# Performance work log

Hardware: AMD Instinct MI355X
Metric: run time of the kernel (lower is better)

Reference implementation:

```python
import jax, jax.numpy as jnp
import numpy as np

NUM_NODES = 40000
NUM_REL = 474
ENT_DIM = 100
REL_DIM = 100
NHID = 100
NHEADS = 2
OUT_DIM = NHID * NHEADS  # 200
ALPHA = 0.2
NUM_ORTHO_HEADS = 2
ORTHO_LAMBDA = 0.01
EPS = 1e-12


def _l2norm(x):
    n = jnp.sqrt(jnp.sum(x * x, axis=1, keepdims=True))
    return x / jnp.maximum(n, EPS)


def _leaky_relu(x):
    return jnp.where(x >= 0, x, ALPHA * x)


def _ortho_loss(a):
    # orthogonality penalty between the NUM_ORTHO_HEADS row-blocks of `a`
    Af = a.reshape(NUM_ORTHO_HEADS, -1)
    Afn = Af / jnp.maximum(jnp.linalg.norm(Af, axis=1, keepdims=True), EPS)
    G = Afn @ Afn.T
    return ORTHO_LAMBDA * jnp.sum((G - jnp.eye(NUM_ORTHO_HEADS, dtype=a.dtype)) ** 2)


def _gat_layer(x, tgt, src, rel, a, a2, concat):
    # x: [N, f]; tgt/src: [E]; rel: [E, r]; a: [out, 2f+r]; a2: [out]
    f = x.shape[1]
    a_t, a_s, a_r = a[:, :f], a[:, f:2 * f], a[:, 2 * f:]
    # edge_m = a @ concat(x[tgt], x[src], rel)^T, computed without materializing the concat
    edge_m = x[tgt] @ a_t.T + x[src] @ a_s.T + rel @ a_r.T  # [E, out]
    powers = -_leaky_relu(edge_m @ a2)  # [E]
    edge_e = jnp.exp(powers)
    rowsum = jax.ops.segment_sum(edge_e, tgt, num_segments=NUM_NODES)  # [N]
    rowsum = jnp.where(rowsum == 0.0, EPS, rowsum)
    h = jax.ops.segment_sum(edge_e[:, None] * edge_m, tgt, num_segments=NUM_NODES)  # [N, out]
    h = h / rowsum[:, None]
    if concat:
        h = jax.nn.elu(h)
    return h, _ortho_loss(a)


def setup_inputs() -> dict:
    key = jax.random.key(0)
    ks = jax.random.split(key, 12)
    E, EN, B = 100000, 30000, 8192
    edge_list = jax.random.randint(ks[0], (2, E), 0, NUM_NODES)
    edge_type = jax.random.randint(ks[1], (E,), 0, NUM_REL)
    batch_inputs = jax.random.randint(ks[2], (B, 3), 0, NUM_REL)  # col 2 < 474 < NUM_NODES, valid node ids
    train_indices_nhop = jax.random.randint(ks[3], (EN, 4), 0, NUM_REL)
    s = 0.1
    entity_embeddings = jax.random.normal(ks[4], (NUM_NODES, ENT_DIM), jnp.float32)
    relation_embeddings = jax.random.normal(ks[5], (NUM_REL, REL_DIM), jnp.float32)
    W_entities = jax.random.normal(ks[6], (ENT_DIM, OUT_DIM), jnp.float32) * s
    W_rel = jax.random.normal(ks[7], (REL_DIM, OUT_DIM), jnp.float32) * s
    att_a = jax.random.normal(ks[8], (NHEADS, NHID, 2 * ENT_DIM + REL_DIM), jnp.float32) * s
    att_a2 = jax.random.normal(ks[9], (NHEADS, NHID), jnp.float32) * s
    out_a = jax.random.normal(ks[10], (OUT_DIM, 3 * OUT_DIM), jnp.float32) * s
    out_a2 = jax.random.normal(ks[11], (OUT_DIM,), jnp.float32) * s
    return {
        'edge_list': edge_list, 'edge_type': edge_type,
        'batch_inputs': batch_inputs, 'train_indices_nhop': train_indices_nhop,
        'entity_embeddings': entity_embeddings, 'relation_embeddings': relation_embeddings,
        'W_entities': W_entities, 'W_rel': W_rel,
        'att_a': att_a, 'att_a2': att_a2, 'out_a': out_a, 'out_a2': out_a2,
    }


def reference(edge_list, edge_type, batch_inputs, train_indices_nhop,
              entity_embeddings, relation_embeddings, W_entities, W_rel,
              att_a, att_a2, out_a, out_a2):
    ent = _l2norm(entity_embeddings)
    # edge lists: aggregation index is edge[0] (target); nhop edges = (col3, col0)
    tgt = jnp.concatenate([edge_list[0], train_indices_nhop[:, 3]])
    src = jnp.concatenate([edge_list[1], train_indices_nhop[:, 0]])
    # layer-1 relation features (1-hop gather + 2-hop sum fusion)
    rel1 = jnp.concatenate([
        relation_embeddings[edge_type],
        relation_embeddings[train_indices_nhop[:, 1]] + relation_embeddings[train_indices_nhop[:, 2]],
    ], axis=0)
    outs = []
    total_ortho = jnp.zeros((), dtype=ent.dtype)
    for i in range(NHEADS):
        h, ol = _gat_layer(ent, tgt, src, rel1, att_a[i], att_a2[i], True)
        outs.append(h)
        total_ortho = total_ortho + ol
    x = jnp.concatenate(outs, axis=1)  # [N, OUT_DIM]  (dropout skipped: eval mode)
    out_relation_1 = relation_embeddings @ W_rel  # [R, OUT_DIM]
    rel2 = jnp.concatenate([
        out_relation_1[edge_type],
        out_relation_1[train_indices_nhop[:, 1]] + out_relation_1[train_indices_nhop[:, 2]],
    ], axis=0)
    x, ol = _gat_layer(x, tgt, src, rel2, out_a, out_a2, False)
    total_ortho = total_ortho + ol
    mask = jnp.zeros((NUM_NODES,), dtype=x.dtype).at[batch_inputs[:, 2]].set(1.0)
    out_entity = ent @ W_entities + mask[:, None] * x
    out_entity = _l2norm(out_entity)
    return out_entity, out_relation_1, total_ortho
```

## Files before the change

### kernel.cpp

```cpp
#include <hip/hip_runtime.h>
#include <cstdint>
#include <cstddef>
#include <math.h>

#define N_NODES 40000
#define N_RELS  474
#define E0      100000
#define NE      130000
#define NB      8192
#define LRALPHA 0.2f

#define KP1 128
#define KP2 256
#define LD1 608
#define LD2 416
#define NPAD1 640
#define NPAD2 448
#define DTH 16

#define M1_L2N   2500
#define M1_HIST  (M1_L2N + 508)
#define M1_UVEC  (M1_HIST + 200)
#define M1_MASK  (M1_UVEC + 32)
#define M1_TOT   (M1_MASK + 128)
#define M2_PACK1 1
#define M2_PACK2 (M2_PACK1 + 320)
#define M2_TOT   (M2_PACK2 + 448)
#define M3_GEMM  508
#define M3_MM    (M3_GEMM + 1250)
#define M3_RELP  (M3_MM + 32)
#define M3_CMP   (M3_RELP + 119)
#define M3_TOT   (M3_CMP + 157)
#define M4_MM    119
#define M4_OFIN  (M4_MM + 32)
#define M4_TOT   (M4_OFIN + 1)
#define N1_MAIN  2500
#define N1_HUB   (N1_MAIN + 512)
#define N1_TOT   (N1_HUB + 119)
#define HUBW     2048
#define N2_MAIN  1250
#define N2_TOT   (N2_MAIN + 512)

typedef __attribute__((ext_vector_type(8))) short short8;
typedef __attribute__((ext_vector_type(4))) float floatx4;

static __device__ __forceinline__ unsigned short f2bf(float f) {
    union { float f; uint32_t u; } v; v.f = f;
    uint32_t r = v.u + 0x7fff + ((v.u >> 16) & 1);
    return (unsigned short)(r >> 16);
}
static __device__ __forceinline__ float bf2f(unsigned short h) {
    union { uint32_t u; float f; } v; v.u = ((uint32_t)h) << 16;
    return v.f;
}
static __device__ __forceinline__ float bflo(uint32_t u) { return bf2f((unsigned short)(u & 0xffff)); }
static __device__ __forceinline__ float bfhi(uint32_t u) { return bf2f((unsigned short)(u >> 16)); }

static __device__ __forceinline__ int rdl(int v, int l) {
    return __builtin_amdgcn_readlane(v, l);
}
static __device__ __forceinline__ float rdlf(float v, int l) {
    return __int_as_float(__builtin_amdgcn_readlane(__float_as_int(v), l));
}
static __device__ __forceinline__ float frcp(float x) { return __builtin_amdgcn_rcpf(x); }


static __device__ void d_l2norm(int bid, int tid, const float* __restrict__ in,
                                unsigned short* __restrict__ out) {
    int wid = (bid * 256 + tid) >> 6;
    int lane = tid & 63;
    int w0 = wid * 4;
    if (w0 >= N_NODES) return;
    int j1 = lane + 64;
    bool v1ok = (j1 < 100);
    float a[4], b[4];
#pragma unroll
    for (int i = 0; i < 4; i++) {
        const float* r = in + (size_t)(w0 + i) * 100;
        a[i] = r[lane];
        b[i] = v1ok ? r[j1] : 0.f;
    }
    float ss[4];
#pragma unroll
    for (int i = 0; i < 4; i++) ss[i] = a[i] * a[i] + b[i] * b[i];
#pragma unroll
    for (int o = 32; o > 0; o >>= 1) {
#pragma unroll
        for (int i = 0; i < 4; i++) ss[i] += __shfl_down(ss[i], o);
    }
#pragma unroll
    for (int i = 0; i < 4; i++) {
        float s = __shfl(ss[i], 0);
        float inv = 1.f / fmaxf(sqrtf(s), 1e-12f);
        unsigned short* dst = out + (size_t)(w0 + i) * KP1;
        dst[lane] = f2bf(a[i] * inv);
        dst[j1] = v1ok ? f2bf(b[i] * inv) : (unsigned short)0;
    }
}

static __device__ void d_hist(int bid, int tid, const int* __restrict__ tgt_el,
                              const int* __restrict__ nhop, int* __restrict__ deg) {
    int e = bid * 256 + tid;
    if (e >= NE) return;
    int t = (e < E0) ? tgt_el[e] : nhop[(size_t)(e - E0) * 4 + 3];
    atomicAdd(&deg[t], 1);
}

static __device__ void d_uvec(int bid, int tid, const float* __restrict__ att_a,
                              const float* __restrict__ att_a2, const float* __restrict__ out_a,
                              const float* __restrict__ out_a2, float* __restrict__ uvecs) {
    int g = (bid * 256 + tid) >> 6;
    int lane = tid & 63;
    if (g >= 800) return;
    float s = 0.f;
    if (g < 400) {
        int v = g / 100, k = g % 100;
        int head = v >> 1, part = v & 1;
        const float* base = att_a + head * 30000 + part * 100 + k;
        const float* a2 = att_a2 + head * 100;
        for (int n = lane; n < 100; n += 64) s += a2[n] * base[n * 300];
    } else {
        int v = (g - 400) / 200, k = (g - 400) % 200;
        const float* base = out_a + v * 200 + k;
        for (int n = lane; n < 200; n += 64) s += out_a2[n] * base[n * 600];
    }
#pragma unroll
    for (int o = 32; o > 0; o >>= 1) s += __shfl_down(s, o);
    if (lane == 0) uvecs[g] = s;
}

static __device__ void d_mask(int bid, int tid, const int* __restrict__ batch,
                              float* __restrict__ mask) {
    int i = bid * 256 + tid;
    if (i < NB) mask[batch[(size_t)i * 3 + 2]] = 1.0f;
}

static __device__ void d_ortho_part(int bid, int tid, const float* __restrict__ att_a,
                                    const float* __restrict__ out_a, float* __restrict__ accum) {
    float loc[9] = {0,0,0,0,0,0,0,0,0};
    for (int i = bid * 256 + tid; i < 90000; i += 128 * 256) {
        int seg, li;
        const float* base;
        int L;
        if (i < 15000)      { seg = 0; li = i;          base = att_a;         L = 15000; }
        else if (i < 30000) { seg = 1; li = i - 15000;  base = att_a + 30000; L = 15000; }
        else                { seg = 2; li = i - 30000;  base = out_a;         L = 60000; }
        float a = base[li], b = base[L + li];
        loc[seg * 3 + 0] += a * a;
        loc[seg * 3 + 1] += b * b;
        loc[seg * 3 + 2] += a * b;
    }
    int lane = tid & 63;
#pragma unroll
    for (int q = 0; q < 9; q++) {
        float s = loc[q];
#pragma unroll
        for (int o = 32; o > 0; o >>= 1) s += __shfl_down(s, o);
        if (lane == 0 && s != 0.f) atomicAdd(&accum[q], s);
    }
}

static __device__ void d_scan2(int tid, int* wtot, int* __restrict__ bsums, int nb) {
    int v = (tid < nb) ? bsums[tid] : 0;
    int lane = tid & 63, wv = tid >> 6;
    int x = v;
#pragma unroll
    for (int o = 1; o < 64; o <<= 1) {
        int t = __shfl_up(x, o);
        if (lane >= o) x += t;
    }
    if (lane == 63) wtot[wv] = x;
    __syncthreads();
    int add = 0;
    for (int k = 0; k < wv; k++) add += wtot[k];
    __syncthreads();
    if (tid < nb) bsums[tid] = add + x - v;
    if (tid == 255) bsums[nb] = add + x;
}

static __device__ void d_pack1(int bid, int tid, const float* __restrict__ att_a,
                               const float* __restrict__ W_ent, const float* __restrict__ uvecs,
                               unsigned short* __restrict__ W) {
    int idx = bid * 256 + tid;
    if (idx >= NPAD1 * KP1) return;
    int j = idx & 7;
    int lane = (idx >> 3) & 63;
    int u = idx >> 9;
    int ks = u & 3;
    int t = u >> 2;
    int r = t * 16 + (lane & 15);
    int k = ks * 32 + (lane >> 4) * 8 + j;
    float val = 0.f;
    if (k < 100) {
        if (r < 200) {
            int i = r >> 1, h = r & 1;
            val = att_a[h * 30000 + i * 300 + k];
        } else if (r < 400) {
            int rr = r - 200, i = rr >> 1, h = rr & 1;
            val = att_a[h * 30000 + i * 300 + 100 + k];
        } else if (r < 600) {
            val = W_ent[k * 200 + (r - 400)];
        } else if (r < 604) {
            val = uvecs[(r - 600) * 100 + k];
        }
    }
    W[idx] = f2bf(val);
}

static __device__ void d_pack2(int bid, int tid, const float* __restrict__ out_a,
                               const float* __restrict__ uvecs, unsigned short* __restrict__ W) {
    int idx = bid * 256 + tid;
    if (idx >= NPAD2 * KP2) return;
    int j = idx & 7;
    int lane = (idx >> 3) & 63;
    int u = idx >> 9;
    int ks = u & 7;
    int t = u >> 3;
    int r = t * 16 + (lane & 15);
    int k = ks * 32 + (lane >> 4) * 8 + j;
    float val = 0.f;
    if (k < 200) {
        int klog = (k & 1) * 100 + (k >> 1);
        if (r < 200)       val = out_a[r * 600 + klog];
        else if (r < 400)  val = out_a[(r - 200) * 600 + 200 + klog];
        else if (r == 400) val = uvecs[400 + klog];
        else if (r == 401) val = uvecs[600 + klog];
    }
    W[idx] = f2bf(val);
}

static __device__ void d_scatter(int bid, int tid, const int* __restrict__ tgt_el,
                                 const int* __restrict__ src_el, const int* __restrict__ etype,
                                 const int* __restrict__ nhop, int* __restrict__ cursor,
                                 int* __restrict__ srcs, int2* __restrict__ relpk) {
    int e = bid * 256 + tid;
    if (e >= NE) return;
    int t, s, r1, r2;
    if (e < E0) {
        t = tgt_el[e]; s = src_el[e]; r1 = etype[e]; r2 = -1;
    } else {
        const int* nh = nhop + (size_t)(e - E0) * 4;
        t = nh[3]; s = nh[0]; r1 = nh[1]; r2 = nh[2];
    }
    int p = atomicAdd(&cursor[t], 1);
    srcs[p] = s;
    relpk[p] = make_int2(r1, r2);
}

static __device__ void d_compact(int bid, int tid, const int* __restrict__ rowptr,
                                 const float* __restrict__ mask,
                                 int* __restrict__ Hlist, int* __restrict__ Mlist,
                                 int* __restrict__ cnts) {
    int i = bid * 256 + tid;
    if (i >= N_NODES) return;
    int deg = rowptr[i + 1] - rowptr[i];
    if (deg > DTH) { int p = atomicAdd(&cnts[0], 1); Hlist[p] = i; }
    if (mask[i] != 0.f) { int p = atomicAdd(&cnts[1], 1); Mlist[p] = i; }
}

template <int KP>
static __device__ void d_gemm(int bx, int by, char* smem_raw, int tid,
                              const unsigned short* __restrict__ A,
                              const unsigned short* __restrict__ B,
                              unsigned short* __restrict__ C,
                              int ldc, int N, int gPerSplit) {
    constexpr int KSTEPS = KP / 32;
    constexpr int KCH = KSTEPS / 4;
    unsigned short (*cbuf)[16][64] = (unsigned short (*)[16][64])smem_raw;
    int wave = tid >> 6;
    int lane = tid & 63;
    int quad = lane >> 4;
    int l16 = lane & 15;
    int m0 = bx * 64 + wave * 16;
    short8 afrag[KSTEPS];
    const unsigned short* arow = A + (size_t)(m0 + l16) * KP + quad * 8;
#pragma unroll
    for (int ks = 0; ks < KSTEPS; ks++)
        afrag[ks] = *(const short8*)(arow + ks * 32);

    int Gtot = (N + 63) >> 6;
    int g0 = by * gPerSplit;
    int g1 = g0 + gPerSplit;
    if (g1 > Gtot) g1 = Gtot;
    for (int g = g0; g < g1; g++) {
        int nb = g << 6;
        const unsigned short* bgrp = B + (((size_t)(g << 2) * KSTEPS) << 9) + (lane << 3);
        floatx4 acc[4];
#pragma unroll
        for (int t = 0; t < 4; t++) acc[t] = (floatx4){0.f, 0.f, 0.f, 0.f};
#pragma unroll
        for (int ch = 0; ch < KCH; ch++) {
            short8 bf[4][4];
#pragma unroll
            for (int t = 0; t < 4; t++)
#pragma unroll
                for (int k = 0; k < 4; k++)
                    bf[t][k] = *(const short8*)(bgrp + ((size_t)(t * KSTEPS + ch * 4 + k) << 9));
#pragma unroll
            for (int k = 0; k < 4; k++)
#pragma unroll
                for (int t = 0; t < 4; t++)
                    acc[t] = __builtin_amdgcn_mfma_f32_16x16x32_bf16(afrag[ch * 4 + k], bf[t][k], acc[t], 0, 0, 0);
        }
        int r0 = quad * 4;
#pragma unroll
        for (int t = 0; t < 4; t++)
#pragma unroll
            for (int i = 0; i < 4; i++)
                cbuf[wave][r0 + i][t * 16 + l16] = f2bf(acc[t][i]);
        int colsA = N - nb; if (colsA > 64) colsA = 64;
        int cols8 = colsA >> 3;
        int sh = (colsA >= 64) ? 3 : 2;
        int nchunks = cols8 << 4;
        for (int c = lane; c < nchunks; c += 64) {
            int row = c >> sh;
            int col8 = (c & (cols8 - 1)) << 3;
            *(uint4*)(C + (size_t)(m0 + row) * ldc + nb + col8) =
                *(const uint4*)&cbuf[wave][row][col8];
        }
    }
}

template <bool BT>
static __device__ void d_mm(int bx, int by, char* smem_raw, int tid,
                            const float* __restrict__ A, int lda,
                            const float* __restrict__ B, int ldb,
                            float* __restrict__ C, int ldc,
                            int M, int N, int K) {
    float (*As)[65] = (float (*)[65])smem_raw;
    float (*Bs)[65] = (float (*)[65])(smem_raw + 16 * 65 * 4);
    int tx = tid & 15, ty = tid >> 4;
    int m0 = by * 64, n0 = bx * 64;
    float acc[4][4] = {};
    for (int k0 = 0; k0 < K; k0 += 16) {
        {
            int r = tid >> 2;
            int c4 = (tid & 3) * 4;
            int m = m0 + r;
#pragma unroll
            for (int u = 0; u < 4; u++) {
                int k = k0 + c4 + u;
                As[c4 + u][r] = (m < M && k < K) ? A[(size_t)m * lda + k] : 0.f;
            }
        }
        if (BT) {
            int r = tid >> 2;
            int c4 = (tid & 3) * 4;
            int n = n0 + r;
#pragma unroll
            for (int u = 0; u < 4; u++) {
                int k = k0 + c4 + u;
                Bs[c4 + u][r] = (n < N && k < K) ? B[(size_t)n * ldb + k] : 0.f;
            }
        } else {
            int kk = tid >> 4;
            int nn4 = (tid & 15) * 4;
            int k = k0 + kk;
#pragma unroll
            for (int u = 0; u < 4; u++) {
                int n = n0 + nn4 + u;
                Bs[kk][nn4 + u] = (k < K && n < N) ? B[(size_t)k * ldb + n] : 0.f;
            }
        }
        __syncthreads();
#pragma unroll
        for (int k = 0; k < 16; k++) {
            float a[4], b[4];
#pragma unroll
            for (int i = 0; i < 4; i++) a[i] = As[k][ty + 16 * i];
#pragma unroll
            for (int j = 0; j < 4; j++) b[j] = Bs[k][tx + 16 * j];
#pragma unroll
            for (int i = 0; i < 4; i++)
#pragma unroll
                for (int j = 0; j < 4; j++) acc[i][j] += a[i] * b[j];
        }
        __syncthreads();
    }
#pragma unroll
    for (int i = 0; i < 4; i++) {
        int m = m0 + ty + 16 * i;
        if (m >= M) continue;
#pragma unroll
        for (int j = 0; j < 4; j++) {
            int n = n0 + tx + 16 * j;
            if (n < N) C[(size_t)m * ldc + n] = acc[i][j];
        }
    }
}

static __device__ void d_relproj1(int bid, int tid, const float* __restrict__ rel_emb,
                                  const float* __restrict__ att_a, float* __restrict__ R1i) {
    int w = (bid * 256 + tid) >> 6;
    int lane = tid & 63;
    if (w >= N_RELS) return;
    const float* re = rel_emb + (size_t)w * 100;
    float2* dst = (float2*)(R1i + (size_t)w * 200);
    for (int f = lane; f < 100; f += 64) {
        const float* a0 = att_a + f * 300 + 200;
        const float* a1 = att_a + 30000 + f * 300 + 200;
// ... 288 lines not shown
        uint32_t sq = *(const uint32_t*)(Qcat + (size_t)sL * LD2 + 400);
        float pp = tdot + bfhi(sq) + dr;
        pp = (pp >= 0.f) ? pp : LRALPHA * pp;
        WL = __expf(-pp);
    }
    float c0 = 0.f, c1 = 0.f, c2 = 0.f, c3 = 0.f;
    float rs = 0.f;
    for (int j = 0; j < fast; j += 4) {
#pragma unroll
        for (int u = 0; u < 4; u++) {
            int jj = j + u;
            bool act = (jj < fast);
            int ls = act ? jj : 0;
            int sE = rdl(sL, ls);
            int rxE = rdl(rxL, ls);
            int ryE = act ? rdl(ryL, ls) : -1;
            float WE = act ? rdlf(WL, ls) : 0.f;
            uint2 qv = make_uint2(0u, 0u);
            float4 rv = make_float4(0.f, 0.f, 0.f, 0.f);
            if (fv) {
                qv = *(const uint2*)(Qcat + (size_t)sE * LD2 + 200 + c4);
                rv = *(const float4*)(R2 + (size_t)rxE * 200 + c4);
                if (ryE >= 0) {
                    float4 rb = *(const float4*)(R2 + (size_t)ryE * 200 + c4);
                    rv.x += rb.x; rv.y += rb.y; rv.z += rb.z; rv.w += rb.w;
                }
            }
            rs += WE;
            c0 += WE * (bflo(qv.x) + rv.x);
            c1 += WE * (bfhi(qv.x) + rv.y);
            c2 += WE * (bflo(qv.y) + rv.z);
            c3 += WE * (bfhi(qv.y) + rv.w);
        }
    }
    for (int p = beg + 64; p < end; p++) {
        int sE = srcs[p];
        int2 rp = relpk[p];
        float dr = dR2[rp.x];
        if (rp.y >= 0) dr += dR2[rp.y];
        uint32_t sq = *(const uint32_t*)(Qcat + (size_t)sE * LD2 + 400);
        float pp = tdot + bfhi(sq) + dr;
        pp = (pp >= 0.f) ? pp : LRALPHA * pp;
        float W = __expf(-pp);
        uint2 qv = make_uint2(0u, 0u);
        float4 rv = make_float4(0.f, 0.f, 0.f, 0.f);
        if (fv) {
            qv = *(const uint2*)(Qcat + (size_t)sE * LD2 + 200 + c4);
            rv = *(const float4*)(R2 + (size_t)rp.x * 200 + c4);
            if (rp.y >= 0) {
                float4 rb = *(const float4*)(R2 + (size_t)rp.y * 200 + c4);
                rv.x += rb.x; rv.y += rb.y; rv.z += rb.z; rv.w += rb.w;
            }
        }
        rs += W;
        c0 += W * (bflo(qv.x) + rv.x);
        c1 += W * (bfhi(qv.x) + rv.y);
        c2 += W * (bflo(qv.y) + rv.z);
        c3 += W * (bfhi(qv.y) + rv.w);
    }
    float d = (rs == 0.f) ? 1e-12f : rs;
    float idn = frcp(d);
    float mk = mask[node];
    float val0 = 0.f, val1 = 0.f, val2 = 0.f, val3 = 0.f;
    if (fv) {
        uint2 t = *(const uint2*)(Qcat + (size_t)node * LD2 + c4);
        uint2 e = *(const uint2*)(Pcat + (size_t)node * LD1 + 400 + c4);
        val0 = bflo(e.x) + mk * ((c0 + rs * bflo(t.x)) * idn);
        val1 = bfhi(e.x) + mk * ((c1 + rs * bfhi(t.x)) * idn);
        val2 = bflo(e.y) + mk * ((c2 + rs * bflo(t.y)) * idn);
        val3 = bfhi(e.y) + mk * ((c3 + rs * bfhi(t.y)) * idn);
    }
    float ss = val0 * val0 + val1 * val1 + val2 * val2 + val3 * val3;
#pragma unroll
    for (int o = 32; o > 0; o >>= 1) ss += __shfl_down(ss, o);
    ss = __shfl(ss, 0);
    float inv = frcp(fmaxf(sqrtf(ss), 1e-12f));
    if (fv) {
        *(float4*)(out + (size_t)node * 200 + c4) =
            make_float4(val0 * inv, val1 * inv, val2 * inv, val3 * inv);
    }
}


__global__ __launch_bounds__(256) void k_mega1(
        const float* __restrict__ ent_emb, unsigned short* __restrict__ ent_bf,
        const int* __restrict__ tgt_el, const int* __restrict__ nhop, int* __restrict__ deg,
        const float* __restrict__ att_a, const float* __restrict__ att_a2,
        const float* __restrict__ out_a, const float* __restrict__ out_a2,
        float* __restrict__ uvecs,
        const int* __restrict__ batch, float* __restrict__ mask, float* __restrict__ oacc) {
    int bid = blockIdx.x, tid = threadIdx.x;
    if (bid < M1_L2N)       d_l2norm(bid, tid, ent_emb, ent_bf);
    else if (bid < M1_HIST) d_hist(bid - M1_L2N, tid, tgt_el, nhop, deg);
    else if (bid < M1_UVEC) d_uvec(bid - M1_HIST, tid, att_a, att_a2, out_a, out_a2, uvecs);
    else if (bid < M1_MASK) d_mask(bid - M1_UVEC, tid, batch, mask);
    else                    d_ortho_part(bid - M1_MASK, tid, att_a, out_a, oacc);
}

__global__ void k_scan1(const int* __restrict__ deg, int* __restrict__ local,
                        int* __restrict__ bsums, int n) {
    int i = blockIdx.x * 256 + threadIdx.x;
    int v = (i < n) ? deg[i] : 0;
    int lane = threadIdx.x & 63;
    int wv = threadIdx.x >> 6;
    int x = v;
#pragma unroll
    for (int o = 1; o < 64; o <<= 1) {
        int t = __shfl_up(x, o);
        if (lane >= o) x += t;
    }
    __shared__ int wtot[4];
    if (lane == 63) wtot[wv] = x;
    __syncthreads();
    int add = 0;
    for (int k = 0; k < wv; k++) add += wtot[k];
    if (i < n) local[i] = add + x - v;
    if (threadIdx.x == 255) bsums[blockIdx.x] = add + x;
}

__global__ __launch_bounds__(256) void k_mega2(
        int* __restrict__ bsums, int nbk,
        const float* __restrict__ att_a, const float* __restrict__ W_ent,
        const float* __restrict__ uvecs, unsigned short* __restrict__ W1,
        const float* __restrict__ out_a, unsigned short* __restrict__ W2) {
    __shared__ int wtot[4];
    int bid = blockIdx.x, tid = threadIdx.x;
    if (bid == 0)            d_scan2(tid, wtot, bsums, nbk);
    else if (bid < M2_PACK2) d_pack1(bid - M2_PACK1, tid, att_a, W_ent, uvecs, W1);
    else                     d_pack2(bid - M2_PACK2, tid, out_a, uvecs, W2);
}

__global__ void k_scan3(const int* __restrict__ local, const int* __restrict__ bsums,
                        int* __restrict__ rowptr, int* __restrict__ cursor, int n, int nb) {
    int i = blockIdx.x * 256 + threadIdx.x;
    if (i < n) {
        int v = local[i] + bsums[blockIdx.x];
        rowptr[i] = v;
        cursor[i] = v;
    } else if (i == n) {
        rowptr[n] = bsums[nb];
    }
}

__global__ __launch_bounds__(256) void k_mega3(
        const int* __restrict__ tgt_el, const int* __restrict__ src_el,
        const int* __restrict__ etype, const int* __restrict__ nhop, int* __restrict__ cursor,
        int* __restrict__ srcs, int2* __restrict__ relpk,
        const unsigned short* __restrict__ ent_bf, const unsigned short* __restrict__ Wcat1,
        unsigned short* __restrict__ Pcat,
        const float* __restrict__ rel_emb, const float* __restrict__ W_rel,
        float* __restrict__ outrel,
        const float* __restrict__ att_a, float* __restrict__ R1i,
        const int* __restrict__ rowptr, const float* __restrict__ mask,
        int* __restrict__ Hlist, int* __restrict__ Mlist, int* __restrict__ cnts) {
    __shared__ __align__(16) char smem[8448];
    int bid = blockIdx.x, tid = threadIdx.x;
    if (bid < M3_GEMM) {
        d_scatter(bid, tid, tgt_el, src_el, etype, nhop, cursor, srcs, relpk);
    } else if (bid < M3_MM) {
        int i = bid - M3_GEMM;
        d_gemm<KP1>(i % 625, i / 625, smem, tid, ent_bf, Wcat1, Pcat, LD1, 608, 5);
    } else if (bid < M3_RELP) {
        int i = bid - M3_MM;
        d_mm<false>(i & 3, i >> 2, smem, tid, rel_emb, 100, W_rel, 200, outrel, 200,
                    N_RELS, 200, 100);
    } else if (bid < M3_CMP) {
        d_relproj1(bid - M3_RELP, tid, rel_emb, att_a, R1i);
    } else {
        d_compact(bid - M3_CMP, tid, rowptr, mask, Hlist, Mlist, cnts);
    }
}

__global__ __launch_bounds__(256) void k_mega4(
        const float* __restrict__ R1i, const float* __restrict__ att_a2,
        float* __restrict__ dR10, float* __restrict__ dR11,
        const float* __restrict__ outrel, const float* __restrict__ out_a,
        float* __restrict__ R2,
        const float* __restrict__ oacc, float* __restrict__ oscalar) {
    __shared__ __align__(16) char smem[8448];
    int bid = blockIdx.x, tid = threadIdx.x;
    if (bid < M4_MM) {
        d_dR1(bid, tid, R1i, att_a2, dR10, dR11);
    } else if (bid < M4_OFIN) {
        int i = bid - M4_MM;
        d_mm<true>(i & 3, i >> 2, smem, tid, outrel, 200, out_a + 400, 600, R2, 200,
                   N_RELS, 200, 200);
    } else {
        d_ortho_fin(tid, oacc, oscalar);
    }
}

__global__ __launch_bounds__(256) void k_gemm2(const unsigned short* __restrict__ A,
                                               const unsigned short* __restrict__ B,
                                               unsigned short* __restrict__ C,
                                               int ldc, int N, int gPerSplit) {
    __shared__ __align__(16) char smem[8192];
    d_gemm<KP2>(blockIdx.x, blockIdx.y, smem, threadIdx.x, A, B, C, ldc, N, gPerSplit);
}

__global__ __launch_bounds__(256, 4) void k_node1(
                        const int* __restrict__ rowptr, const int* __restrict__ srcs,
                        const int2* __restrict__ relpk,
                        const unsigned short* __restrict__ Pcat,
                        const float* __restrict__ R1i,
                        const float* __restrict__ dR10, const float* __restrict__ dR11,
                        unsigned short* __restrict__ x,
                        const int* __restrict__ Hlist, const int* __restrict__ cnts,
                        const float* __restrict__ R2, const float* __restrict__ out_a2,
                        float* __restrict__ dR2) {
    int bid = blockIdx.x, tid = threadIdx.x;
    int lane = tid & 63;
    if (bid < N1_MAIN) {
        int wid = __builtin_amdgcn_readfirstlane(bid * 4 + (tid >> 6));
        d_node1_main(wid, lane, rowptr, srcs, relpk, Pcat, R1i, dR10, dR11, x);
    } else if (bid < N1_HUB) {
        int hw = (bid - N1_MAIN) * 4 + (tid >> 6);
        int cnt = cnts[0];
        for (int j = hw; j < cnt; j += HUBW) {
            int node = __builtin_amdgcn_readfirstlane(Hlist[j]);
            d_node1_one(node, lane, rowptr, srcs, relpk, Pcat, R1i, dR10, dR11, x);
        }
    } else {
        int w = (bid - N1_HUB) * 4 + (tid >> 6);
        if (w < N_RELS) {
            const float* r = R2 + (size_t)w * 200;
            float s = 0.f;
            for (int j = lane; j < 200; j += 64) s += r[j] * out_a2[j];
#pragma unroll
            for (int o = 32; o > 0; o >>= 1) s += __shfl_down(s, o);
            if (lane == 0) dR2[w] = s;
        }
    }
}

__global__ __launch_bounds__(256, 4) void k_node2(
                        const int* __restrict__ rowptr, const int* __restrict__ srcs,
                        const int2* __restrict__ relpk,
                        const unsigned short* __restrict__ Qcat,
                        const unsigned short* __restrict__ Pcat,
                        const float* __restrict__ R2, const float* __restrict__ dR2,
                        const float* __restrict__ mask,
                        const int* __restrict__ Mlist, const int* __restrict__ cnts,
                        float* __restrict__ out) {
    int bid = blockIdx.x, tid = threadIdx.x;
    int lane = tid & 63;
    if (bid < N2_MAIN) {
        int wid = __builtin_amdgcn_readfirstlane(bid * 4 + (tid >> 6));
        int n0 = wid * 8;
        bool fv = (lane < 50);
        int c4 = lane * 4;
        float mval = (lane < 8) ? mask[n0 + lane] : 0.f;
        uint2 e[8];
#pragma unroll
        for (int i = 0; i < 8; i++)
            e[i] = fv ? *(const uint2*)(Pcat + (size_t)(n0 + i) * LD1 + 400 + c4)
                      : make_uint2(0u, 0u);
#pragma unroll
        for (int i = 0; i < 8; i++) {
            if (rdlf(mval, i) != 0.f) continue;
            float v0 = bflo(e[i].x), v1 = bfhi(e[i].x);
            float v2 = bflo(e[i].y), v3 = bfhi(e[i].y);
            float ss = v0 * v0 + v1 * v1 + v2 * v2 + v3 * v3;
#pragma unroll
            for (int o = 32; o > 0; o >>= 1) ss += __shfl_down(ss, o);
            ss = __shfl(ss, 0);
            float inv = frcp(fmaxf(sqrtf(ss), 1e-12f));
            if (fv) {
                *(float4*)(out + (size_t)(n0 + i) * 200 + c4) =
                    make_float4(v0 * inv, v1 * inv, v2 * inv, v3 * inv);
            }
        }
    } else {
        int hw = (bid - N2_MAIN) * 4 + (tid >> 6);
        int cnt = cnts[1];
        for (int j = hw; j < cnt; j += HUBW) {
            int node = __builtin_amdgcn_readfirstlane(Mlist[j]);
            d_node2_one(node, lane, rowptr, srcs, relpk, Qcat, Pcat, R2, dR2, mask, out);
        }
    }
}

extern "C" void kernel_launch(void* const* d_in, const int* in_sizes, int n_in,
                              void* d_out, int out_size, void* d_ws, size_t ws_size,
                              hipStream_t stream) {
    const int* edge_list = (const int*)d_in[0];
    const int* edge_type = (const int*)d_in[1];
    const int* batch     = (const int*)d_in[2];
    const int* nhop      = (const int*)d_in[3];
    const float* ent_emb = (const float*)d_in[4];
    const float* rel_emb = (const float*)d_in[5];
    const float* W_ent   = (const float*)d_in[6];
    const float* W_rel   = (const float*)d_in[7];
    const float* att_a   = (const float*)d_in[8];
    const float* att_a2  = (const float*)d_in[9];
    const float* out_a   = (const float*)d_in[10];
    const float* out_a2  = (const float*)d_in[11];
    float* out = (float*)d_out;
    const int* tgt_el = edge_list;
    const int* src_el = edge_list + E0;

    char* ws = (char*)d_ws;
    size_t o = 0;
    auto alloc = [&](size_t nbytes) -> char* {
        char* p = ws + o;
        o += (nbytes + 255) & ~(size_t)255;
        return p;
    };
    unsigned short* ent_bf  = (unsigned short*)alloc((size_t)N_NODES * KP1 * 2);
    unsigned short* x_bf    = (unsigned short*)alloc((size_t)N_NODES * KP2 * 2);
    unsigned short* Pcat    = (unsigned short*)alloc((size_t)N_NODES * LD1 * 2);
    unsigned short* Qcat    = (unsigned short*)alloc((size_t)N_NODES * LD2 * 2);
    unsigned short* Wcat1   = (unsigned short*)alloc((size_t)NPAD1 * KP1 * 2);
    unsigned short* Wcat2   = (unsigned short*)alloc((size_t)NPAD2 * KP2 * 2);
    float* uvecs = (float*)alloc(800 * 4);
    float* R1i   = (float*)alloc(474u * 200 * 4);
    float* R2    = (float*)alloc(474u * 200 * 4);
    float* dR10  = (float*)alloc(474u * 4);
    float* dR11  = (float*)alloc(474u * 4);
    float* dR2   = (float*)alloc(474u * 4);
    int* rowptr  = (int*)alloc((N_NODES + 1) * 4);
    int* cursor  = (int*)alloc(N_NODES * 4);
    int* srcs    = (int*)alloc((size_t)NE * 4);
    int2* relpk  = (int2*)alloc((size_t)NE * 8);
    float* mask  = (float*)alloc(N_NODES * 4);
    int* scanloc = (int*)alloc(N_NODES * 4);
    int* bsums   = (int*)alloc(260 * 4);
    float* oacc  = (float*)alloc(9 * 4);
    int* Hlist   = (int*)alloc(N_NODES * 4);
    int* Mlist   = (int*)alloc(N_NODES * 4);
    int* cnts    = (int*)alloc(2 * 4);

    hipMemsetAsync(cursor, 0, N_NODES * 4, stream);
    hipMemsetAsync(mask, 0, N_NODES * 4, stream);
    hipMemsetAsync(oacc, 0, 9 * 4, stream);
    hipMemsetAsync(cnts, 0, 2 * 4, stream);

    k_mega1<<<M1_TOT, 256, 0, stream>>>(ent_emb, ent_bf, tgt_el, nhop, cursor,
                                        att_a, att_a2, out_a, out_a2, uvecs,
                                        batch, mask, oacc);
    k_scan1<<<157, 256, 0, stream>>>(cursor, scanloc, bsums, N_NODES);
    k_mega2<<<M2_TOT, 256, 0, stream>>>(bsums, 157, att_a, W_ent, uvecs, Wcat1, out_a, Wcat2);
    k_scan3<<<157, 256, 0, stream>>>(scanloc, bsums, rowptr, cursor, N_NODES, 157);
    k_mega3<<<M3_TOT, 256, 0, stream>>>(tgt_el, src_el, edge_type, nhop, cursor,
                                        srcs, relpk, ent_bf, Wcat1, Pcat,
                                        rel_emb, W_rel, out + 8000000, att_a, R1i,
                                        rowptr, mask, Hlist, Mlist, cnts);
    k_mega4<<<M4_TOT, 256, 0, stream>>>(R1i, att_a2, dR10, dR11,
                                        out + 8000000, out_a, R2, oacc, out + 8094800);
    k_node1<<<N1_TOT, 256, 0, stream>>>(rowptr, srcs, relpk, Pcat, R1i, dR10, dR11,
                                        x_bf, Hlist, cnts, R2, out_a2, dR2);
    k_gemm2<<<dim3(625, 2), 256, 0, stream>>>(x_bf, Wcat2, Qcat, LD2, 416, 4);
    k_node2<<<N2_TOT, 256, 0, stream>>>(rowptr, srcs, relpk, Qcat, Pcat, R2, dR2,
                                        mask, Mlist, cnts, out);
}
```

Before: 342.8 us.

## Fuse L2-normalization into layer-1 GEMM and restructure launch schedule

The separate entity L2-norm pass and its bf16 buffer are removed. The layer-1 GEMM now loads fp32 rows, normalizes them in shared memory and converts to bf16 fragments inline, computing 64 rows per block instead of the earlier tiling. The uvec dot products move into the weight-pack stages, and the relation GEMMs and dR1 move earlier so the megakernels can be rebalanced and one launch dropped. The unmasked output normalization moves into the node1 launch. The risk is redundant per-thread dot-product loops in the pack stages and a GEMM tile shape that may be less efficient.

```diff
diff --git a/kernel.cpp b/kernel.cpp
--- a/kernel.cpp
+++ b/kernel.cpp
@@ -17,29 +17,25 @@
 #define NPAD1 640
 #define NPAD2 448
 #define DTH 16
-
-#define M1_L2N   2500
-#define M1_HIST  (M1_L2N + 508)
-#define M1_UVEC  (M1_HIST + 200)
-#define M1_MASK  (M1_UVEC + 32)
-#define M1_TOT   (M1_MASK + 128)
-#define M2_PACK1 1
-#define M2_PACK2 (M2_PACK1 + 320)
-#define M2_TOT   (M2_PACK2 + 448)
-#define M3_GEMM  508
-#define M3_MM    (M3_GEMM + 1250)
-#define M3_RELP  (M3_MM + 32)
-#define M3_CMP   (M3_RELP + 119)
-#define M3_TOT   (M3_CMP + 157)
-#define M4_MM    119
-#define M4_OFIN  (M4_MM + 32)
-#define M4_TOT   (M4_OFIN + 1)
+#define HUBW 2048
+
+#define A_HIST   508
+#define A_RELP   (A_HIST + 119)
+#define A_MMW    (A_RELP + 32)
+#define A_PACK1  (A_MMW + 320)
+#define A_PACK2  (A_PACK1 + 448)
+#define A_MASK   (A_PACK2 + 32)
+#define A_TOT    (A_MASK + 128)
+#define B_DR1    120
+#define B_TOT    (B_DR1 + 32)
+#define C_SCAT   508
+#define C_GEMM   (C_SCAT + 1250)
+#define C_CMP    (C_GEMM + 157)
+#define C_DOTV   (C_CMP + 119)
+#define C_TOT    (C_DOTV + 1)
 #define N1_MAIN  2500
 #define N1_HUB   (N1_MAIN + 512)
-#define N1_TOT   (N1_HUB + 119)
-#define HUBW     2048
-#define N2_MAIN  1250
-#define N2_TOT   (N2_MAIN + 512)
+#define N1_TOT   (N1_HUB + 1250)
 
 typedef __attribute__((ext_vector_type(8))) short short8;
 typedef __attribute__((ext_vector_type(4))) float floatx4;
@@ -64,39 +60,6 @@
 }
 static __device__ __forceinline__ float frcp(float x) { return __builtin_amdgcn_rcpf(x); }
 
-
-static __device__ void d_l2norm(int bid, int tid, const float* __restrict__ in,
-                                unsigned short* __restrict__ out) {
-    int wid = (bid * 256 + tid) >> 6;
-    int lane = tid & 63;
-    int w0 = wid * 4;
-    if (w0 >= N_NODES) return;
-    int j1 = lane + 64;
-    bool v1ok = (j1 < 100);
-    float a[4], b[4];
-#pragma unroll
-    for (int i = 0; i < 4; i++) {
-        const float* r = in + (size_t)(w0 + i) * 100;
-        a[i] = r[lane];
-        b[i] = v1ok ? r[j1] : 0.f;
-    }
-    float ss[4];
-#pragma unroll
-    for (int i = 0; i < 4; i++) ss[i] = a[i] * a[i] + b[i] * b[i];
-#pragma unroll
-    for (int o = 32; o > 0; o >>= 1) {
-#pragma unroll
-        for (int i = 0; i < 4; i++) ss[i] += __shfl_down(ss[i], o);
-    }
-#pragma unroll
-    for (int i = 0; i < 4; i++) {
-        float s = __shfl(ss[i], 0);
-        float inv = 1.f / fmaxf(sqrtf(s), 1e-12f);
-        unsigned short* dst = out + (size_t)(w0 + i) * KP1;
-        dst[lane] = f2bf(a[i] * inv);
-        dst[j1] = v1ok ? f2bf(b[i] * inv) : (unsigned short)0;
-    }
-}
 
 static __device__ void d_hist(int bid, int tid, const int* __restrict__ tgt_el,
                               const int* __restrict__ nhop, int* __restrict__ deg) {
@@ -104,29 +67,6 @@
     if (e >= NE) return;
     int t = (e < E0) ? tgt_el[e] : nhop[(size_t)(e - E0) * 4 + 3];
     atomicAdd(&deg[t], 1);
-}
-
-static __device__ void d_uvec(int bid, int tid, const float* __restrict__ att_a,
-                              const float* __restrict__ att_a2, const float* __restrict__ out_a,
-                              const float* __restrict__ out_a2, float* __restrict__ uvecs) {
-    int g = (bid * 256 + tid) >> 6;
-    int lane = tid & 63;
-    if (g >= 800) return;
-    float s = 0.f;
-    if (g < 400) {
-        int v = g / 100, k = g % 100;
-        int head = v >> 1, part = v & 1;
-        const float* base = att_a + head * 30000 + part * 100 + k;
-        const float* a2 = att_a2 + head * 100;
-        for (int n = lane; n < 100; n += 64) s += a2[n] * base[n * 300];
-    } else {
-        int v = (g - 400) / 200, k = (g - 400) % 200;
-        const float* base = out_a + v * 200 + k;
-        for (int n = lane; n < 200; n += 64) s += out_a2[n] * base[n * 600];
-    }
-#pragma unroll
-    for (int o = 32; o > 0; o >>= 1) s += __shfl_down(s, o);
-    if (lane == 0) uvecs[g] = s;
 }
 
 static __device__ void d_mask(int bid, int tid, const int* __restrict__ batch,
@@ -179,7 +119,8 @@
 }
 
 static __device__ void d_pack1(int bid, int tid, const float* __restrict__ att_a,
-                               const float* __restrict__ W_ent, const float* __restrict__ uvecs,
+                               const float* __restrict__ att_a2,
+                               const float* __restrict__ W_ent,
                                unsigned short* __restrict__ W) {
     int idx = bid * 256 + tid;
     if (idx >= NPAD1 * KP1) return;
@@ -201,14 +142,20 @@
         } else if (r < 600) {
             val = W_ent[k * 200 + (r - 400)];
         } else if (r < 604) {
-            val = uvecs[(r - 600) * 100 + k];
+            int v = r - 600, head = v >> 1, part = v & 1;
+            const float* base = att_a + head * 30000 + part * 100 + k;
+            const float* a2v = att_a2 + head * 100;
+            float s = 0.f;
+            for (int n = 0; n < 100; n++) s += a2v[n] * base[n * 300];
+            val = s;
         }
     }
     W[idx] = f2bf(val);
 }
 
 static __device__ void d_pack2(int bid, int tid, const float* __restrict__ out_a,
-                               const float* __restrict__ uvecs, unsigned short* __restrict__ W) {
+                               const float* __restrict__ out_a2,
+                               unsigned short* __restrict__ W) {
     int idx = bid * 256 + tid;
     if (idx >= NPAD2 * KP2) return;
     int j = idx & 7;
@@ -223,8 +170,15 @@
         int klog = (k & 1) * 100 + (k >> 1);
         if (r < 200)       val = out_a[r * 600 + klog];
         else if (r < 400)  val = out_a[(r - 200) * 600 + 200 + klog];
-        else if (r == 400) val = uvecs[400 + klog];
-        else if (r == 401) val = uvecs[600 + klog];
+        else if (r == 400) {
+            float s = 0.f;
+            for (int n = 0; n < 200; n++) s += out_a2[n] * out_a[n * 600 + klog];
+            val = s;
+        } else if (r == 401) {
+            float s = 0.f;
+            for (int n = 0; n < 200; n++) s += out_a2[n] * out_a[n * 600 + 200 + klog];
+            val = s;
+        }
     }
     W[idx] = f2bf(val);
 }
@@ -316,6 +270,87 @@
             int row = c >> sh;
             int col8 = (c & (cols8 - 1)) << 3;
             *(uint4*)(C + (size_t)(m0 + row) * ldc + nb + col8) =
+                *(const uint4*)&cbuf[wave][row][col8];
+        }
+    }
+}
+
+static __device__ void d_gemm1f(int bx, int by, char* smem_raw, int tid,
+                                const float* __restrict__ ent,
+                                const unsigned short* __restrict__ B,
+                                unsigned short* __restrict__ C) {
+    float (*rows)[105] = (float (*)[105])smem_raw;
+    float* invn = (float*)(smem_raw + 64 * 105 * 4);
+    int m0 = bx * 64;
+    for (int idx = tid; idx < 6400; idx += 256) {
+        int r = idx / 100, c = idx - r * 100;
+        rows[r][c] = ent[(size_t)(m0 + r) * 100 + c];
+    }
+    __syncthreads();
+    {
+        int r = tid >> 2, q = tid & 3;
+        const float* rp = rows[r] + q * 25;
+        float s = 0.f;
+#pragma unroll
+        for (int c = 0; c < 25; c++) { float v = rp[c]; s += v * v; }
+        s += __shfl_xor(s, 1);
+        s += __shfl_xor(s, 2);
+        if (q == 0) invn[r] = 1.f / fmaxf(sqrtf(s), 1e-12f);
+    }
+    __syncthreads();
+    int wave = tid >> 6;
+    int lane = tid & 63;
+    int quad = lane >> 4;
+    int l16 = lane & 15;
+    int rr = wave * 16 + l16;
+    float inv = invn[rr];
+    short8 afrag[4];
+#pragma unroll
+    for (int ks = 0; ks < 4; ks++) {
+        short8 f;
+#pragma unroll
+        for (int j = 0; j < 8; j++) {
+            int col = ks * 32 + quad * 8 + j;
+            f[j] = (col < 100) ? (short)f2bf(rows[rr][col] * inv) : (short)0;
+        }
+        afrag[ks] = f;
+    }
+    __syncthreads();
+    unsigned short (*cbuf)[16][64] = (unsigned short (*)[16][64])smem_raw;
+    int mo0 = m0 + wave * 16;
+    int g0 = by * 5, g1 = g0 + 5;
+    if (g1 > 10) g1 = 10;
+    for (int g = g0; g < g1; g++) {
+        int nb = g << 6;
+        const unsigned short* bgrp = B + (((size_t)(g << 2) * 4) << 9) + (lane << 3);
+        floatx4 acc[4];
+#pragma unroll
+        for (int t = 0; t < 4; t++) acc[t] = (floatx4){0.f, 0.f, 0.f, 0.f};
+        short8 bf[4][4];
+#pragma unroll
+        for (int t = 0; t < 4; t++)
+#pragma unroll
+            for (int k = 0; k < 4; k++)
+                bf[t][k] = *(const short8*)(bgrp + ((size_t)(t * 4 + k) << 9));
+#pragma unroll
+        for (int k = 0; k < 4; k++)
+#pragma unroll
+            for (int t = 0; t < 4; t++)
+                acc[t] = __builtin_amdgcn_mfma_f32_16x16x32_bf16(afrag[k], bf[t][k], acc[t], 0, 0, 0);
+        int r0 = quad * 4;
+#pragma unroll
+        for (int t = 0; t < 4; t++)
+#pragma unroll
+            for (int i = 0; i < 4; i++)
+                cbuf[wave][r0 + i][t * 16 + l16] = f2bf(acc[t][i]);
+        int colsA = 608 - nb; if (colsA > 64) colsA = 64;
+        int cols8 = colsA >> 3;
+        int sh = (colsA >= 64) ? 3 : 2;
+        int nchunks = cols8 << 4;
+        for (int c = lane; c < nchunks; c += 64) {
+            int row = c >> sh;
+            int col8 = (c & (cols8 - 1)) << 3;
+            *(uint4*)(C + (size_t)(mo0 + row) * LD1 + nb + col8) =
                 *(const uint4*)&cbuf[wave][row][col8];
         }
     }
@@ -770,19 +805,35 @@
 }
 
 
-__global__ __launch_bounds__(256) void k_mega1(
-        const float* __restrict__ ent_emb, unsigned short* __restrict__ ent_bf,
+__global__ __launch_bounds__(256) void k_megaA(
         const int* __restrict__ tgt_el, const int* __restrict__ nhop, int* __restrict__ deg,
-        const float* __restrict__ att_a, const float* __restrict__ att_a2,
+        const float* __restrict__ rel_emb, const float* __restrict__ att_a,
+        float* __restrict__ R1i,
+        const float* __restrict__ W_rel, float* __restrict__ outrel,
+        const float* __restrict__ att_a2, const float* __restrict__ W_ent,
+        unsigned short* __restrict__ W1,
         const float* __restrict__ out_a, const float* __restrict__ out_a2,
-        float* __restrict__ uvecs,
+        unsigned short* __restrict__ W2,
         const int* __restrict__ batch, float* __restrict__ mask, float* __restrict__ oacc) {
+    __shared__ __align__(16) char smem[8448];
     int bid = blockIdx.x, tid = threadIdx.x;
-    if (bid < M1_L2N)       d_l2norm(bid, tid, ent_emb, ent_bf);
-    else if (bid < M1_HIST) d_hist(bid - M1_L2N, tid, tgt_el, nhop, deg);
-    else if (bid < M1_UVEC) d_uvec(bid - M1_HIST, tid, att_a, att_a2, out_a, out_a2, uvecs);
-    else if (bid < M1_MASK) d_mask(bid - M1_UVEC, tid, batch, mask);
-    else                    d_ortho_part(bid - M1_MASK, tid, att_a, out_a, oacc);
+    if (bid < A_HIST) {
+        d_hist(bid, tid, tgt_el, nhop, deg);
+    } else if (bid < A_RELP) {
+        d_relproj1(bid - A_HIST, tid, rel_emb, att_a, R1i);
+    } else if (bid < A_MMW) {
+        int i = bid - A_RELP;
+        d_mm<false>(i & 3, i >> 2, smem, tid, rel_emb, 100, W_rel, 200, outrel, 200,
+                    N_RELS, 200, 100);
+    } else if (bid < A_PACK1) {
+        d_pack1(bid - A_MMW, tid, att_a, att_a2, W_ent, W1);
+    } else if (bid < A_PACK2) {
+        d_pack2(bid - A_PACK1, tid, out_a, out_a2, W2);
+    } else if (bid < A_MASK) {
+        d_mask(bid - A_PACK2, tid, batch, mask);
+    } else {
+        d_ortho_part(bid - A_MASK, tid, att_a, out_a, oacc);
+    }
 }
 
 __global__ void k_scan1(const int* __restrict__ deg, int* __restrict__ local,
@@ -806,16 +857,24 @@
     if (threadIdx.x == 255) bsums[blockIdx.x] = add + x;
 }
 
-__global__ __launch_bounds__(256) void k_mega2(
+__global__ __launch_bounds__(256) void k_megaB(
         int* __restrict__ bsums, int nbk,
-        const float* __restrict__ att_a, const float* __restrict__ W_ent,
-        const float* __restrict__ uvecs, unsigned short* __restrict__ W1,
-        const float* __restrict__ out_a, unsigned short* __restrict__ W2) {
+        const float* __restrict__ R1i, const float* __restrict__ att_a2,
+        float* __restrict__ dR10, float* __restrict__ dR11,
+        const float* __restrict__ outrel, const float* __restrict__ out_a,
+        float* __restrict__ R2) {
+    __shared__ __align__(16) char smem[8448];
     __shared__ int wtot[4];
     int bid = blockIdx.x, tid = threadIdx.x;
-    if (bid == 0)            d_scan2(tid, wtot, bsums, nbk);
-    else if (bid < M2_PACK2) d_pack1(bid - M2_PACK1, tid, att_a, W_ent, uvecs, W1);
-    else                     d_pack2(bid - M2_PACK2, tid, out_a, uvecs, W2);
+    if (bid == 0) {
+        d_scan2(tid, wtot, bsums, nbk);
+    } else if (bid < B_DR1) {
+        d_dR1(bid - 1, tid, R1i, att_a2, dR10, dR11);
+    } else {
+        int i = bid - B_DR1;
+        d_mm<true>(i & 3, i >> 2, smem, tid, outrel, 200, out_a + 400, 600, R2, 200,
+                   N_RELS, 200, 200);
+    }
 }
 
 __global__ void k_scan3(const int* __restrict__ local, const int* __restrict__ bsums,
@@ -830,60 +889,40 @@
     }
 }
 
-__global__ __launch_bounds__(256) void k_mega3(
+__global__ __launch_bounds__(256) void k_megaC(
         const int* __restrict__ tgt_el, const int* __restrict__ src_el,
         const int* __restrict__ etype, const int* __restrict__ nhop, int* __restrict__ cursor,
         int* __restrict__ srcs, int2* __restrict__ relpk,
-        const unsigned short* __restrict__ ent_bf, const unsigned short* __restrict__ Wcat1,
+        const float* __restrict__ ent_emb, const unsigned short* __restrict__ Wcat1,
         unsigned short* __restrict__ Pcat,
-        const float* __restrict__ rel_emb, const float* __restrict__ W_rel,
-        float* __restrict__ outrel,
-        const float* __restrict__ att_a, float* __restrict__ R1i,
         const int* __restrict__ rowptr, const float* __restrict__ mask,
-        int* __restrict__ Hlist, int* __restrict__ Mlist, int* __restrict__ cnts) {
-    __shared__ __align__(16) char smem[8448];
+        int* __restrict__ Hlist, int* __restrict__ Mlist, int* __restrict__ cnts,
+        const float* __restrict__ R2, const float* __restrict__ out_a2,
+        float* __restrict__ dR2,
+        const float* __restrict__ oacc, float* __restrict__ oscalar) {
+    __shared__ __align__(16) char smem[27392];
     int bid = blockIdx.x, tid = threadIdx.x;
-    if (bid < M3_GEMM) {
+    if (bid < C_SCAT) {
         d_scatter(bid, tid, tgt_el, src_el, etype, nhop, cursor, srcs, relpk);
-    } else if (bid < M3_MM) {
-        int i = bid - M3_GEMM;
-        d_gemm<KP1>(i % 625, i / 625, smem, tid, ent_bf, Wcat1, Pcat, LD1, 608, 5);
-    } else if (bid < M3_RELP) {
-        int i = bid - M3_MM;
-        d_mm<false>(i & 3, i >> 2, smem, tid, rel_emb, 100, W_rel, 200, outrel, 200,
-                    N_RELS, 200, 100);
-    } else if (bid < M3_CMP) {
-        d_relproj1(bid - M3_RELP, tid, rel_emb, att_a, R1i);
-    } else {
-        d_compact(bid - M3_CMP, tid, rowptr, mask, Hlist, Mlist, cnts);
-    }
-}
-
-__global__ __launch_bounds__(256) void k_mega4(
-        const float* __restrict__ R1i, const float* __restrict__ att_a2,
-        float* __restrict__ dR10, float* __restrict__ dR11,
-        const float* __restrict__ outrel, const float* __restrict__ out_a,
-        float* __restrict__ R2,
-        const float* __restrict__ oacc, float* __restrict__ oscalar) {
-    __shared__ __align__(16) char smem[8448];
-    int bid = blockIdx.x, tid = threadIdx.x;
-    if (bid < M4_MM) {
-        d_dR1(bid, tid, R1i, att_a2, dR10, dR11);
-    } else if (bid < M4_OFIN) {
-        int i = bid - M4_MM;
-        d_mm<true>(i & 3, i >> 2, smem, tid, outrel, 200, out_a + 400, 600, R2, 200,
-                   N_RELS, 200, 200);
+    } else if (bid < C_GEMM) {
+        int i = bid - C_SCAT;
+        d_gemm1f(i % 625, i / 625, smem, tid, ent_emb, Wcat1, Pcat);
+    } else if (bid < C_CMP) {
+        d_compact(bid - C_GEMM, tid, rowptr, mask, Hlist, Mlist, cnts);
+    } else if (bid < C_DOTV) {
+        int w = (bid - C_CMP) * 4 + (tid >> 6);
+        int lane = tid & 63;
+        if (w < N_RELS) {
+            const float* r = R2 + (size_t)w * 200;
+            float s = 0.f;
+            for (int j = lane; j < 200; j += 64) s += r[j] * out_a2[j];
+#pragma unroll
+            for (int o = 32; o > 0; o >>= 1) s += __shfl_down(s, o);
+            if (lane == 0) dR2[w] = s;
+        }
     } else {
         d_ortho_fin(tid, oacc, oscalar);
     }
-}
-
-__global__ __launch_bounds__(256) void k_gemm2(const unsigned short* __restrict__ A,
-                                               const unsigned short* __restrict__ B,
-                                               unsigned short* __restrict__ C,
-                                               int ldc, int N, int gPerSplit) {
-    __shared__ __align__(16) char smem[8192];
-    d_gemm<KP2>(blockIdx.x, blockIdx.y, smem, threadIdx.x, A, B, C, ldc, N, gPerSplit);
 }
 
 __global__ __launch_bounds__(256, 4) void k_node1(
@@ -894,8 +933,7 @@
                         const float* __restrict__ dR10, const float* __restrict__ dR11,
                         unsigned short* __restrict__ x,
                         const int* __restrict__ Hlist, const int* __restrict__ cnts,
-                        const float* __restrict__ R2, const float* __restrict__ out_a2,
-                        float* __restrict__ dR2) {
+                        const float* __restrict__ mask, float* __restrict__ out) {
     int bid = blockIdx.x, tid = threadIdx.x;
     int lane = tid & 63;
     if (bid < N1_MAIN) {
@@ -909,19 +947,43 @@
             d_node1_one(node, lane, rowptr, srcs, relpk, Pcat, R1i, dR10, dR11, x);
         }
     } else {
-        int w = (bid - N1_HUB) * 4 + (tid >> 6);
-        if (w < N_RELS) {
-            const float* r = R2 + (size_t)w * 200;
-            float s = 0.f;
-            for (int j = lane; j < 200; j += 64) s += r[j] * out_a2[j];
-#pragma unroll
-            for (int o = 32; o > 0; o >>= 1) s += __shfl_down(s, o);
-            if (lane == 0) dR2[w] = s;
-        }
-    }
-}
-
-__global__ __launch_bounds__(256, 4) void k_node2(
+        int wid = __builtin_amdgcn_readfirstlane((bid - N1_HUB) * 4 + (tid >> 6));
+        int n0 = wid * 8;
+        bool fv = (lane < 50);
+        int c4 = lane * 4;
+        float mval = (lane < 8) ? mask[n0 + lane] : 0.f;
+        uint2 e[8];
+#pragma unroll
+        for (int i = 0; i < 8; i++)
+            e[i] = fv ? *(const uint2*)(Pcat + (size_t)(n0 + i) * LD1 + 400 + c4)
+                      : make_uint2(0u, 0u);
+#pragma unroll
+        for (int i = 0; i < 8; i++) {
+            if (rdlf(mval, i) != 0.f) continue;
+            float v0 = bflo(e[i].x), v1 = bfhi(e[i].x);
+            float v2 = bflo(e[i].y), v3 = bfhi(e[i].y);
+            float ss = v0 * v0 + v1 * v1 + v2 * v2 + v3 * v3;
+#pragma unroll
+            for (int o = 32; o > 0; o >>= 1) ss += __shfl_down(ss, o);
+            ss = __shfl(ss, 0);
+            float inv = frcp(fmaxf(sqrtf(ss), 1e-12f));
+            if (fv) {
+                *(float4*)(out + (size_t)(n0 + i) * 200 + c4) =
+                    make_float4(v0 * inv, v1 * inv, v2 * inv, v3 * inv);
+            }
+        }
+    }
+}
+
+__global__ __launch_bounds__(256) void k_gemm2(const unsigned short* __restrict__ A,
+                                               const unsigned short* __restrict__ B,
+                                               unsigned short* __restrict__ C,
+                                               int ldc, int N, int gPerSplit) {
+    __shared__ __align__(16) char smem[8192];
+    d_gemm<KP2>(blockIdx.x, blockIdx.y, smem, threadIdx.x, A, B, C, ldc, N, gPerSplit);
+}
+
+__global__ __launch_bounds__(256, 4) void k_node2h(
                         const int* __restrict__ rowptr, const int* __restrict__ srcs,
                         const int2* __restrict__ relpk,
                         const unsigned short* __restrict__ Qcat,
@@ -930,41 +992,13 @@
                         const float* __restrict__ mask,
                         const int* __restrict__ Mlist, const int* __restrict__ cnts,
                         float* __restrict__ out) {
-    int bid = blockIdx.x, tid = threadIdx.x;
+    int tid = threadIdx.x;
     int lane = tid & 63;
-    if (bid < N2_MAIN) {
-        int wid = __builtin_amdgcn_readfirstlane(bid * 4 + (tid >> 6));
-        int n0 = wid * 8;
-        bool fv = (lane < 50);
-        int c4 = lane * 4;
-        float mval = (lane < 8) ? mask[n0 + lane] : 0.f;
-        uint2 e[8];
-#pragma unroll
-        for (int i = 0; i < 8; i++)
-            e[i] = fv ? *(const uint2*)(Pcat + (size_t)(n0 + i) * LD1 + 400 + c4)
-                      : make_uint2(0u, 0u);
-#pragma unroll
-        for (int i = 0; i < 8; i++) {
-            if (rdlf(mval, i) != 0.f) continue;
-            float v0 = bflo(e[i].x), v1 = bfhi(e[i].x);
-            float v2 = bflo(e[i].y), v3 = bfhi(e[i].y);
-            float ss = v0 * v0 + v1 * v1 + v2 * v2 + v3 * v3;
-#pragma unroll
-            for (int o = 32; o > 0; o >>= 1) ss += __shfl_down(ss, o);
-            ss = __shfl(ss, 0);
-            float inv = frcp(fmaxf(sqrtf(ss), 1e-12f));
-            if (fv) {
-                *(float4*)(out + (size_t)(n0 + i) * 200 + c4) =
-                    make_float4(v0 * inv, v1 * inv, v2 * inv, v3 * inv);
-            }
-        }
-    } else {
-        int hw = (bid - N2_MAIN) * 4 + (tid >> 6);
-        int cnt = cnts[1];
-        for (int j = hw; j < cnt; j += HUBW) {
-            int node = __builtin_amdgcn_readfirstlane(Mlist[j]);
-            d_node2_one(node, lane, rowptr, srcs, relpk, Qcat, Pcat, R2, dR2, mask, out);
-        }
+    int hw = blockIdx.x * 4 + (tid >> 6);
+    int cnt = cnts[1];
+    for (int j = hw; j < cnt; j += HUBW) {
+        int node = __builtin_amdgcn_readfirstlane(Mlist[j]);
+        d_node2_one(node, lane, rowptr, srcs, relpk, Qcat, Pcat, R2, dR2, mask, out);
     }
 }
 
@@ -994,13 +1028,11 @@
         o += (nbytes + 255) & ~(size_t)255;
         return p;
     };
-    unsigned short* ent_bf  = (unsigned short*)alloc((size_t)N_NODES * KP1 * 2);
     unsigned short* x_bf    = (unsigned short*)alloc((size_t)N_NODES * KP2 * 2);
     unsigned short* Pcat    = (unsigned short*)alloc((size_t)N_NODES * LD1 * 2);
     unsigned short* Qcat    = (unsigned short*)alloc((size_t)N_NODES * LD2 * 2);
     unsigned short* Wcat1   = (unsigned short*)alloc((size_t)NPAD1 * KP1 * 2);
     unsigned short* Wcat2   = (unsigned short*)alloc((size_t)NPAD2 * KP2 * 2);
-    float* uvecs = (float*)alloc(800 * 4);
     float* R1i   = (float*)alloc(474u * 200 * 4);
     float* R2    = (float*)alloc(474u * 200 * 4);
     float* dR10  = (float*)alloc(474u * 4);
@@ -1023,21 +1055,23 @@
     hipMemsetAsync(oacc, 0, 9 * 4, stream);
     hipMemsetAsync(cnts, 0, 2 * 4, stream);
 
-    k_mega1<<<M1_TOT, 256, 0, stream>>>(ent_emb, ent_bf, tgt_el, nhop, cursor,
-                                        att_a, att_a2, out_a, out_a2, uvecs,
-                                        batch, mask, oacc);
+    k_megaA<<<A_TOT, 256, 0, stream>>>(tgt_el, nhop, cursor,
+                                       rel_emb, att_a, R1i,
+                                       W_rel, out + 8000000,
+                                       att_a2, W_ent, Wcat1,
+                                       out_a, out_a2, Wcat2,
+                                       batch, mask, oacc);
     k_scan1<<<157, 256, 0, stream>>>(cursor, scanloc, bsums, N_NODES);
-    k_mega2<<<M2_TOT, 256, 0, stream>>>(bsums, 157, att_a, W_ent, uvecs, Wcat1, out_a, Wcat2);
+    k_megaB<<<B_TOT, 256, 0, stream>>>(bsums, 157, R1i, att_a2, dR10, dR11,
+                                       out + 8000000, out_a, R2);
     k_scan3<<<157, 256, 0, stream>>>(scanloc, bsums, rowptr, cursor, N_NODES, 157);
-    k_mega3<<<M3_TOT, 256, 0, stream>>>(tgt_el, src_el, edge_type, nhop, cursor,
-                                        srcs, relpk, ent_bf, Wcat1, Pcat,
-                                        rel_emb, W_rel, out + 8000000, att_a, R1i,
-                                        rowptr, mask, Hlist, Mlist, cnts);
-    k_mega4<<<M4_TOT, 256, 0, stream>>>(R1i, att_a2, dR10, dR11,
-                                        out + 8000000, out_a, R2, oacc, out + 8094800);
+    k_megaC<<<C_TOT, 256, 0, stream>>>(tgt_el, src_el, edge_type, nhop, cursor,
+                                       srcs, relpk, ent_emb, Wcat1, Pcat,
+                                       rowptr, mask, Hlist, Mlist, cnts,
+                                       R2, out_a2, dR2, oacc, out + 8094800);
     k_node1<<<N1_TOT, 256, 0, stream>>>(rowptr, srcs, relpk, Pcat, R1i, dR10, dR11,
-                                        x_bf, Hlist, cnts, R2, out_a2, dR2);
+                                        x_bf, Hlist, cnts, mask, out);
     k_gemm2<<<dim3(625, 2), 256, 0, stream>>>(x_bf, Wcat2, Qcat, LD2, 416, 4);
-    k_node2<<<N2_TOT, 256, 0, stream>>>(rowptr, srcs, relpk, Qcat, Pcat, R2, dR2,
-                                        mask, Mlist, cnts, out);
-}
+    k_node2h<<<512, 256, 0, stream>>>(rowptr, srcs, relpk, Qcat, Pcat, R2, dR2,
+                                      mask, Mlist, cnts, out);
+}
```

Measured after the change: 326.9 us. 4.6% less time.
